# Performance work log

Hardware: AMD Instinct MI355X
Metric: run time of the kernel (lower is better)

## Reference

```python
import jax, jax.numpy as jnp
import numpy as np

H = 32       # num query heads
KVH = 8      # num kv heads
D = 2048     # hidden_dim
B = 2
S = 2048
HD = D // H  # head_dim = 64


def setup_inputs() -> dict:
    key = jax.random.key(0)
    ks = jax.random.split(key, 9)
    s = 1.0 / np.sqrt(D).astype(np.float32)
    kvd = KVH * HD
    x = jax.random.normal(ks[0], (B, S, D), jnp.float32)
    # weights stored as (in, out) so forward is x @ W + b
    Wq = jax.random.normal(ks[1], (D, D), jnp.float32) * s
    bq = jax.random.normal(ks[2], (D,), jnp.float32) * 0.01
    Wk = jax.random.normal(ks[3], (D, kvd), jnp.float32) * s
    bk = jax.random.normal(ks[4], (kvd,), jnp.float32) * 0.01
    Wv = jax.random.normal(ks[5], (D, kvd), jnp.float32) * s
    bv = jax.random.normal(ks[6], (kvd,), jnp.float32) * 0.01
    Wo = jax.random.normal(ks[7], (D, D), jnp.float32) * s
    bo = jax.random.normal(ks[8], (D,), jnp.float32) * 0.01
    return {"x": x, "Wq": Wq, "bq": bq, "Wk": Wk, "bk": bk,
            "Wv": Wv, "bv": bv, "Wo": Wo, "bo": bo}


def reference(x, Wq, bq, Wk, bk, Wv, bv, Wo, bo):
    b, s, d = x.shape
    hd = d // H
    # projections -> (B, heads, S, head_dim)
    Q = (x @ Wq + bq).reshape(b, s, H, hd).transpose(0, 2, 1, 3)
    K = (x @ Wk + bk).reshape(b, s, KVH, hd).transpose(0, 2, 1, 3)
    V = (x @ Wv + bv).reshape(b, s, KVH, hd).transpose(0, 2, 1, 3)
    # GQA: repeat KV heads to match query heads (repeat_interleave on head dim)
    rep = H // KVH
    Kr = jnp.repeat(K, rep, axis=1)
    Vr = jnp.repeat(V, rep, axis=1)
    scale = jnp.asarray(1.0 / np.sqrt(hd), x.dtype)
    scores = jnp.einsum('bhqd,bhkd->bhqk', Q, Kr) * scale
    attn = jax.nn.softmax(scores, axis=-1)
    out = jnp.einsum('bhqk,bhkd->bhqd', attn, Vr)
    out = out.transpose(0, 2, 1, 3).reshape(b, s, d)
    return out @ Wo + bo
```

## Files before the change

### kernel.cpp

```cpp
#include <hip/hip_runtime.h>
#include <hip/hip_bf16.h>
#include <cstdint>

#define NH 32
#define NKVH 8
#define DM 2048
#define NB 2
#define SQ 2048
#define HDIM 64
#define MT (NB*SQ)
#define KVD (NKVH*HDIM)

typedef __attribute__((ext_vector_type(8))) short short8;
typedef __attribute__((ext_vector_type(4))) short short4v;
typedef __attribute__((ext_vector_type(4))) float f32x4;
typedef __attribute__((ext_vector_type(16))) float f32x16;
typedef __attribute__((ext_vector_type(4))) unsigned int uint4v;

static __device__ __forceinline__ short f2b(float f) {
  uint32_t u = __builtin_bit_cast(uint32_t, f);
  u += 0x7FFFu + ((u >> 16) & 1u);
  return (short)(u >> 16);
}

#define GLL16(g, l) __builtin_amdgcn_global_load_lds(                          \
    (__attribute__((address_space(1))) const void*)(g),                        \
    (__attribute__((address_space(3))) void*)(l), 16, 0, 0)

__global__ void cast_x_kernel(const float* __restrict__ x, short* __restrict__ xb, int n4) {
  int i = blockIdx.x * blockDim.x + threadIdx.x;
  const int stride = gridDim.x * blockDim.x;
  for (; i < n4; i += stride) {
    const float4 v = ((const float4*)x)[i];
    short4v o;
    o.x = f2b(v.x); o.y = f2b(v.y); o.z = f2b(v.z); o.w = f2b(v.w);
    ((short4v*)xb)[i] = o;
  }
}

__global__ void transpose_cast_kernel(const float* __restrict__ W, short* __restrict__ Wt,
                                      int Kd, int Nd) {
  __shared__ float tile[32][33];
  const int n0 = blockIdx.x * 32, k0 = blockIdx.y * 32;
  const int tx = threadIdx.x & 31, ty = threadIdx.x >> 5;
#pragma unroll
  for (int i = 0; i < 4; i++)
    tile[ty + i * 8][tx] = W[(size_t)(k0 + ty + i * 8) * Nd + n0 + tx];
  __syncthreads();
#pragma unroll
  for (int i = 0; i < 4; i++)
    Wt[(size_t)(n0 + ty + i * 8) * Kd + k0 + tx] = f2b(tile[tx][ty + i * 8]);
}

template <int EPI>
__global__ __launch_bounds__(256) void gemm_kernel(const short* __restrict__ A,
                                                   const short* __restrict__ Bt,
                                                   const float* __restrict__ bias,
                                                   void* __restrict__ Cout, int N) {
  __shared__ __align__(16) short As[128 * 32];
  __shared__ __align__(16) short Bs[128 * 32];
  const int K = DM;
  const int tid = threadIdx.x;
  const int wave = tid >> 6, lane = tid & 63;
  const int g = lane >> 4, r16 = lane & 15;
  const int m0 = blockIdx.y * 128, n0 = blockIdx.x * 128;
  const int wr = wave >> 1, wc = wave & 1;

  f32x4 acc[4][4];
#pragma unroll
  for (int i = 0; i < 4; i++)
#pragma unroll
    for (int j = 0; j < 4; j++) acc[i][j] = (f32x4){0.f, 0.f, 0.f, 0.f};

  const int srow = lane >> 2, sslot = lane & 3;
  const short* aS0 = A + (size_t)(m0 + (wave * 2 + 0) * 16 + srow) * K + sslot * 8;
  const short* aS1 = A + (size_t)(m0 + (wave * 2 + 1) * 16 + srow) * K + sslot * 8;
  const short* bS0 = Bt + (size_t)(n0 + (wave * 2 + 0) * 16 + srow) * K + sslot * 8;
  const short* bS1 = Bt + (size_t)(n0 + (wave * 2 + 1) * 16 + srow) * K + sslot * 8;
  short* aD0 = As + (wave * 2 + 0) * 512;
  short* aD1 = As + (wave * 2 + 1) * 512;
  short* bD0 = Bs + (wave * 2 + 0) * 512;
  short* bD1 = Bs + (wave * 2 + 1) * 512;

  for (int k0 = 0; k0 < K; k0 += 32) {
    GLL16(aS0 + k0, aD0);
    GLL16(aS1 + k0, aD1);
    GLL16(bS0 + k0, bD0);
    GLL16(bS1 + k0, bD1);
    __syncthreads();
    short8 af[4], bf[4];
#pragma unroll
    for (int mi = 0; mi < 4; mi++)
      af[mi] = *(const short8*)&As[(wr * 64 + mi * 16 + r16) * 32 + g * 8];
#pragma unroll
    for (int ni = 0; ni < 4; ni++)
      bf[ni] = *(const short8*)&Bs[(wc * 64 + ni * 16 + r16) * 32 + g * 8];
#pragma unroll
    for (int mi = 0; mi < 4; mi++)
#pragma unroll
      for (int ni = 0; ni < 4; ni++)
        acc[mi][ni] = __builtin_amdgcn_mfma_f32_16x16x32_bf16(af[mi], bf[ni], acc[mi][ni], 0, 0, 0);
    __syncthreads();
  }

  float bvv[4];
#pragma unroll
  for (int ni = 0; ni < 4; ni++) bvv[ni] = bias[n0 + wc * 64 + ni * 16 + r16];
#pragma unroll
  for (int mi = 0; mi < 4; mi++) {
#pragma unroll
    for (int ni = 0; ni < 4; ni++) {
      const int n = n0 + wc * 64 + ni * 16 + r16;
#pragma unroll
      for (int j = 0; j < 4; j++) {
        const int m = m0 + wr * 64 + mi * 16 + g * 4 + j;
        const float v = acc[mi][ni][j] + bvv[ni];
        if (EPI == 0) {
          ((short*)Cout)[(size_t)m * N + n] = f2b(v);
        } else {
          ((float*)Cout)[(size_t)m * N + n] = v;
        }
      }
    }
  }
}

__global__ __launch_bounds__(256) void gemm_kv_kernel(const short* __restrict__ A,
                                                      const short* __restrict__ Bt,
                                                      const float* __restrict__ bk,
                                                      const float* __restrict__ bv,
                                                      short* __restrict__ Kout,
                                                      short* __restrict__ Vout) {
  __shared__ __align__(16) short As[128 * 32];
  __shared__ __align__(16) short Bs[128 * 32];
  const int K = DM;
  const int tid = threadIdx.x;
  const int wave = tid >> 6, lane = tid & 63;
  const int g = lane >> 4, r16 = lane & 15;
  const int m0 = blockIdx.y * 128, n0 = blockIdx.x * 128;
  const int wr = wave >> 1, wc = wave & 1;

  f32x4 acc[4][4];
#pragma unroll
  for (int i = 0; i < 4; i++)
#pragma unroll
    for (int j = 0; j < 4; j++) acc[i][j] = (f32x4){0.f, 0.f, 0.f, 0.f};

  const int srow = lane >> 2, sslot = lane & 3;
  const short* aS0 = A + (size_t)(m0 + (wave * 2 + 0) * 16 + srow) * K + sslot * 8;
  const short* aS1 = A + (size_t)(m0 + (wave * 2 + 1) * 16 + srow) * K + sslot * 8;
  const short* bS0 = Bt + (size_t)(n0 + (wave * 2 + 0) * 16 + srow) * K + sslot * 8;
  const short* bS1 = Bt + (size_t)(n0 + (wave * 2 + 1) * 16 + srow) * K + sslot * 8;
  short* aD0 = As + (wave * 2 + 0) * 512;
  short* aD1 = As + (wave * 2 + 1) * 512;
  short* bD0 = Bs + (wave * 2 + 0) * 512;
  short* bD1 = Bs + (wave * 2 + 1) * 512;

  for (int k0 = 0; k0 < K; k0 += 32) {
    GLL16(aS0 + k0, aD0);
    GLL16(aS1 + k0, aD1);
    GLL16(bS0 + k0, bD0);
    GLL16(bS1 + k0, bD1);
    __syncthreads();
    short8 af[4], bf[4];
#pragma unroll
    for (int mi = 0; mi < 4; mi++)
      af[mi] = *(const short8*)&As[(wr * 64 + mi * 16 + r16) * 32 + g * 8];
#pragma unroll
    for (int ni = 0; ni < 4; ni++)
      bf[ni] = *(const short8*)&Bs[(wc * 64 + ni * 16 + r16) * 32 + g * 8];
#pragma unroll
    for (int mi = 0; mi < 4; mi++)
#pragma unroll
      for (int ni = 0; ni < 4; ni++)
        acc[mi][ni] = __builtin_amdgcn_mfma_f32_16x16x32_bf16(af[mi], bf[ni], acc[mi][ni], 0, 0, 0);
    __syncthreads();
  }

  const bool isK = (n0 < 512);
  float bvv[4];
#pragma unroll
  for (int ni = 0; ni < 4; ni++) {
    const int n = n0 + wc * 64 + ni * 16 + r16;
    bvv[ni] = isK ? bk[n] : bv[n - 512];
  }
#pragma unroll
  for (int mi = 0; mi < 4; mi++) {
#pragma unroll
    for (int ni = 0; ni < 4; ni++) {
      const int n = n0 + wc * 64 + ni * 16 + r16;
#pragma unroll
      for (int j = 0; j < 4; j++) {
        const int m = m0 + wr * 64 + mi * 16 + g * 4 + j;
        const float v = acc[mi][ni][j] + bvv[ni];
        if (isK) {
          Kout[(size_t)m * KVD + n] = f2b(v);
        } else {
          const int np = n - 512;
          const int bb = m >> 11, s = m & (SQ - 1);
          const int kvh = np >> 6, d = np & 63;
          Vout[((size_t)((bb * NKVH + kvh) * HDIM + d) << 11) + s] = f2b(v);
        }
      }
    }
  }
}

__global__ __launch_bounds__(256, 2) void attn_kernel(const short* __restrict__ Qb,
                                                      const short* __restrict__ Kb,
                                                      const short* __restrict__ Vtb,
                                                      short* __restrict__ Ab) {
  __shared__ __align__(16) short Ks[2][64 * 64];
  __shared__ __align__(16) short Vs[2][64 * 64];
  __shared__ float alds[4][32];

  const int tid = threadIdx.x, wave = tid >> 6, lane = tid & 63;
  const int la31 = lane & 31, hi = lane >> 5;

  const int pb = blockIdx.x;
  const int lb = (pb & 7) * 128 + (pb >> 3);
  const int qb = lb & 15, h = (lb >> 4) & 31, b = lb >> 9;
  const int kvh = h >> 2;

  const float SCL = 0.18033688f;
  const float THR = 44.3614f;

  short8 qf[4];
  {
    const int qrow = b * SQ + qb * 128 + wave * 32 + la31;
    const short* qp = Qb + (size_t)qrow * DM + h * HDIM;
#pragma unroll
    for (int ks = 0; ks < 4; ks++)
      qf[ks] = *(const short8*)(qp + ks * 16 + hi * 8);
  }

  f32x16 o[2];
#pragma unroll
  for (int nt = 0; nt < 2; nt++)
#pragma unroll
    for (int r = 0; r < 16; r++) o[nt][r] = 0.f;
  float m = -1e30f, l = 0.f;

  const int r3 = lane >> 3, sp = lane & 7;
  const int cs = (sp ^ r3) * 8;
  const int krow0 = wave * 16 + r3, krow1 = wave * 16 + 8 + r3;
  const short* kS0 = Kb + (size_t)(b * SQ + krow0) * KVD + kvh * HDIM + cs;
  const short* kS1 = Kb + (size_t)(b * SQ + krow1) * KVD + kvh * HDIM + cs;
  const short* vS0 = Vtb + (size_t)((b * NKVH + kvh) * HDIM + krow0) * SQ + cs;
  const short* vS1 = Vtb + (size_t)((b * NKVH + kvh) * HDIM + krow1) * SQ + cs;
  char* kD0base = (char*)&Ks[0][0] + (wave * 2 + 0) * 1024;
  char* kD1base = (char*)&Ks[0][0] + (wave * 2 + 1) * 1024;
  char* vD0base = (char*)&Vs[0][0] + (wave * 2 + 0) * 1024;
  char* vD1base = (char*)&Vs[0][0] + (wave * 2 + 1) * 1024;

  const int xr = (la31 & 7) << 4;

  GLL16(kS0, kD0base);
  GLL16(kS1, kD1base);
  GLL16(vS0, vD0base);
  GLL16(vS1, vD1base);
  __syncthreads();

  int cur = 0;
  for (int t = 0; t < SQ / 64; t++) {
    if (t + 1 < SQ / 64) {
      const int nxt = cur ^ 1;
      const size_t ko = (size_t)(t + 1) * 64 * KVD;
      const int vo = (t + 1) * 64;
      GLL16(kS0 + ko, kD0base + nxt * 8192);
      GLL16(kS1 + ko, kD1base + nxt * 8192);
      GLL16(vS0 + vo, vD0base + nxt * 8192);
      GLL16(vS1 + vo, vD1base + nxt * 8192);
    }

    f32x16 st[2];
#pragma unroll
    for (int tt = 0; tt < 2; tt++) {
#pragma unroll
      for (int r = 0; r < 16; r++) st[tt][r] = 0.f;
#pragma unroll
      for (int ks = 0; ks < 4; ks++) {
        const short8 kf = *(const short8*)((const char*)&Ks[cur][0] +
            (32 * tt + la31) * 128 + ((32 * ks + 16 * hi) ^ xr));
        st[tt] = __builtin_amdgcn_mfma_f32_32x32x16_bf16(kf, qf[ks], st[tt], 0, 0, 0);
      }
    }

    float t16a[16];
#pragma unroll
    for (int i = 0; i < 16; i++) t16a[i] = fmaxf(st[0][i], st[1][i]);
#pragma unroll
    for (int off = 8; off >= 1; off >>= 1)
#pragma unroll
      for (int i = 0; i < off; i++) t16a[i] = fmaxf(t16a[i], t16a[i + off]);
    float pmax = t16a[0];
    pmax = fmaxf(pmax, __shfl_xor(pmax, 32));

    if (!__all(pmax <= m + THR)) {
      const float mnew = fmaxf(m, pmax);
      const float al = exp2f((m - mnew) * SCL);
      m = mnew;
      l *= al;
      alds[wave][la31] = al;
      asm volatile("s_waitcnt lgkmcnt(0)" ::: "memory");
      f32x4 av[4];
#pragma unroll
      for (int rr = 0; rr < 4; rr++)
        av[rr] = *(const f32x4*)&alds[wave][rr * 8 + hi * 4];
#pragma unroll
      for (int nt = 0; nt < 2; nt++)
#pragma unroll
        for (int r = 0; r < 16; r++) o[nt][r] *= av[r >> 2][r & 3];
    }

    const float nmsc = -m * SCL;
#pragma unroll
    for (int tt = 0; tt < 2; tt++)
#pragma unroll
      for (int r = 0; r < 16; r++)
        st[tt][r] = exp2f(fmaf(st[tt][r], SCL, nmsc));

    {
      float u[16];
#pragma unroll
      for (int i = 0; i < 16; i++) u[i] = st[0][i] + st[1][i];
#pragma unroll
      for (int off = 8; off >= 1; off >>= 1)
#pragma unroll
        for (int i = 0; i < off; i++) u[i] += u[i + off];
      float ps = u[0];
      ps += __shfl_xor(ps, 32);
      l += ps;
    }

    uint32_t pk[16];
#pragma unroll
    for (int tt = 0; tt < 2; tt++)
#pragma unroll
      for (int i = 0; i < 8; i++)
        pk[tt * 8 + i] = ((uint32_t)(uint16_t)f2b(st[tt][2 * i + 1]) << 16) |
                         (uint16_t)f2b(st[tt][2 * i]);

    short8 pa[4];
#pragma unroll
    for (int ks4 = 0; ks4 < 4; ks4++) {
      uint32_t w02[2], w13[2];
#pragma unroll
      for (int pp = 0; pp < 2; pp++) {
        const uint32_t a = pk[ks4 * 4 + pp];
        const uint32_t c = pk[ks4 * 4 + 2 + pp];
        const uint32_t u = hi ? a : c;
        const uint32_t s2 = (uint32_t)__shfl_xor((int)u, 32);
        w02[pp] = hi ? s2 : a;
        w13[pp] = hi ? c : s2;
      }
      uint4v wv;
      wv.x = w02[0]; wv.y = w02[1]; wv.z = w13[0]; wv.w = w13[1];
      pa[ks4] = __builtin_bit_cast(short8, wv);
    }

#pragma unroll
    for (int nt = 0; nt < 2; nt++)
#pragma unroll
      for (int ks = 0; ks < 4; ks++) {
        const short8 vf = *(const short8*)((const char*)&Vs[cur][0] +
            (32 * nt + la31) * 128 + ((32 * ks + 16 * hi) ^ xr));
        o[nt] = __builtin_amdgcn_mfma_f32_32x32x16_bf16(pa[ks], vf, o[nt], 0, 0, 0);
      }

    __syncthreads();
    cur ^= 1;
  }

  alds[wave][la31] = l;
  asm volatile("s_waitcnt lgkmcnt(0)" ::: "memory");
  float inv[16];
#pragma unroll
  for (int rr = 0; rr < 4; rr++) {
    const f32x4 lv = *(const f32x4*)&alds[wave][rr * 8 + hi * 4];
#pragma unroll
    for (int j = 0; j < 4; j++) inv[rr * 4 + j] = 1.0f / lv[j];
  }
  const int orow = b * SQ + qb * 128 + wave * 32;
#pragma unroll
  for (int nt = 0; nt < 2; nt++)
#pragma unroll
    for (int r = 0; r < 16; r++) {
      const int q = (r & 3) + 8 * (r >> 2) + 4 * hi;
      Ab[(size_t)(orow + q) * DM + h * HDIM + nt * 32 + la31] =
          f2b(o[nt][r] * inv[(r >> 2) * 4 + (r & 3)]);
    }
}

extern "C" void kernel_launch(void* const* d_in, const int* in_sizes, int n_in,
                              void* d_out, int out_size, void* d_ws, size_t ws_size,
                              hipStream_t stream) {
  const float* x  = (const float*)d_in[0];
  const float* Wq = (const float*)d_in[1];
  const float* bq = (const float*)d_in[2];
  const float* Wk = (const float*)d_in[3];
  const float* bk = (const float*)d_in[4];
  const float* Wv = (const float*)d_in[5];
  const float* bv = (const float*)d_in[6];
  const float* Wo = (const float*)d_in[7];
  const float* bo = (const float*)d_in[8];

  short* ws = (short*)d_ws;
  size_t off = 0;
  short* xb  = ws + off; off += (size_t)MT * DM;
  short* Wqt = ws + off; off += (size_t)DM * DM;
  short* Wkt = ws + off; off += (size_t)KVD * DM;
  short* Wvt = ws + off; off += (size_t)KVD * DM;
  short* Wot = ws + off; off += (size_t)DM * DM;
  short* Qb  = ws + off; off += (size_t)MT * DM;
  short* Kb  = ws + off; off += (size_t)MT * KVD;
  short* Vtb = ws + off; off += (size_t)MT * KVD;
  short* Ab  = ws + off;

  cast_x_kernel<<<2048, 256, 0, stream>>>(x, xb, MT * DM / 4);
  transpose_cast_kernel<<<dim3(DM / 32, DM / 32), 256, 0, stream>>>(Wq, Wqt, DM, DM);
  transpose_cast_kernel<<<dim3(KVD / 32, DM / 32), 256, 0, stream>>>(Wk, Wkt, DM, KVD);
  transpose_cast_kernel<<<dim3(KVD / 32, DM / 32), 256, 0, stream>>>(Wv, Wvt, DM, KVD);
  transpose_cast_kernel<<<dim3(DM / 32, DM / 32), 256, 0, stream>>>(Wo, Wot, DM, DM);

  gemm_kernel<0><<<dim3(DM / 128, MT / 128), 256, 0, stream>>>(xb, Wqt, bq, Qb, DM);
  gemm_kv_kernel<<<dim3(1024 / 128, MT / 128), 256, 0, stream>>>(xb, Wkt, bk, bv, Kb, Vtb);

  attn_kernel<<<NB * NH * (SQ / 128), 256, 0, stream>>>(Qb, Kb, Vtb, Ab);

  gemm_kernel<2><<<dim3(DM / 128, MT / 128), 256, 0, stream>>>(Ab, Wot, bo, d_out, DM);
}
```

Before: 419.3 us.

## Double-buffer GEMM LDS tiles, add setprio around MFMA, use packed bf16 convert

The projection GEMMs now double-buffer their LDS tiles, prefetching the next K-slice with global_load_lds while computing the current one. This removes one barrier per iteration and overlaps load latency with MFMA work. s_setprio raises wave priority around MFMA blocks in both the GEMM and attention kernels. In attention, the row-max reduction is rewritten as a flatter tree, and P is packed with the hardware v_cvt_pk_bf16_f32 instruction instead of software rounding. Double buffering doubles LDS use per block, which may lower occupancy, and the hardware convert's rounding may differ slightly from the manual f2b.

Result: faster. 395.5 us (-5.7%).

```diff
diff --git a/kernel.cpp b/kernel.cpp
--- a/kernel.cpp
+++ b/kernel.cpp
@@ -23,6 +23,12 @@
   return (short)(u >> 16);
 }
 
+static __device__ __forceinline__ uint32_t cvt_pk_bf16(float lo, float hi) {
+  uint32_t r;
+  asm("v_cvt_pk_bf16_f32 %0, %1, %2" : "=v"(r) : "v"(lo), "v"(hi));
+  return r;
+}
+
 #define GLL16(g, l) __builtin_amdgcn_global_load_lds(                          \
     (__attribute__((address_space(1))) const void*)(g),                        \
     (__attribute__((address_space(3))) void*)(l), 16, 0, 0)
@@ -57,8 +63,8 @@
                                                    const short* __restrict__ Bt,
                                                    const float* __restrict__ bias,
                                                    void* __restrict__ Cout, int N) {
-  __shared__ __align__(16) short As[128 * 32];
-  __shared__ __align__(16) short Bs[128 * 32];
+  __shared__ __align__(16) short As[2 * 128 * 32];
+  __shared__ __align__(16) short Bs[2 * 128 * 32];
   const int K = DM;
   const int tid = threadIdx.x;
   const int wave = tid >> 6, lane = tid & 63;
@@ -82,25 +88,39 @@
   short* bD0 = Bs + (wave * 2 + 0) * 512;
   short* bD1 = Bs + (wave * 2 + 1) * 512;
 
+  GLL16(aS0, aD0);
+  GLL16(aS1, aD1);
+  GLL16(bS0, bD0);
+  GLL16(bS1, bD1);
+  __syncthreads();
+
+  int buf = 0;
   for (int k0 = 0; k0 < K; k0 += 32) {
-    GLL16(aS0 + k0, aD0);
-    GLL16(aS1 + k0, aD1);
-    GLL16(bS0 + k0, bD0);
-    GLL16(bS1 + k0, bD1);
-    __syncthreads();
+    if (k0 + 32 < K) {
+      const int nb2 = (buf ^ 1) * 4096;
+      GLL16(aS0 + k0 + 32, aD0 + nb2);
+      GLL16(aS1 + k0 + 32, aD1 + nb2);
+      GLL16(bS0 + k0 + 32, bD0 + nb2);
+      GLL16(bS1 + k0 + 32, bD1 + nb2);
+    }
+    const short* Ac = As + buf * 4096;
+    const short* Bc = Bs + buf * 4096;
     short8 af[4], bf[4];
 #pragma unroll
     for (int mi = 0; mi < 4; mi++)
-      af[mi] = *(const short8*)&As[(wr * 64 + mi * 16 + r16) * 32 + g * 8];
+      af[mi] = *(const short8*)&Ac[(wr * 64 + mi * 16 + r16) * 32 + g * 8];
 #pragma unroll
     for (int ni = 0; ni < 4; ni++)
-      bf[ni] = *(const short8*)&Bs[(wc * 64 + ni * 16 + r16) * 32 + g * 8];
+      bf[ni] = *(const short8*)&Bc[(wc * 64 + ni * 16 + r16) * 32 + g * 8];
+    __builtin_amdgcn_s_setprio(1);
 #pragma unroll
     for (int mi = 0; mi < 4; mi++)
 #pragma unroll
       for (int ni = 0; ni < 4; ni++)
         acc[mi][ni] = __builtin_amdgcn_mfma_f32_16x16x32_bf16(af[mi], bf[ni], acc[mi][ni], 0, 0, 0);
+    __builtin_amdgcn_s_setprio(0);
     __syncthreads();
+    buf ^= 1;
   }
 
   float bvv[4];
@@ -131,8 +151,8 @@
                                                       const float* __restrict__ bv,
                                                       short* __restrict__ Kout,
                                                       short* __restrict__ Vout) {
-  __shared__ __align__(16) short As[128 * 32];
-  __shared__ __align__(16) short Bs[128 * 32];
+  __shared__ __align__(16) short As[2 * 128 * 32];
+  __shared__ __align__(16) short Bs[2 * 128 * 32];
   const int K = DM;
   const int tid = threadIdx.x;
   const int wave = tid >> 6, lane = tid & 63;
@@ -156,25 +176,39 @@
   short* bD0 = Bs + (wave * 2 + 0) * 512;
   short* bD1 = Bs + (wave * 2 + 1) * 512;
 
+  GLL16(aS0, aD0);
+  GLL16(aS1, aD1);
+  GLL16(bS0, bD0);
+  GLL16(bS1, bD1);
+  __syncthreads();
+
+  int buf = 0;
   for (int k0 = 0; k0 < K; k0 += 32) {
-    GLL16(aS0 + k0, aD0);
-    GLL16(aS1 + k0, aD1);
-    GLL16(bS0 + k0, bD0);
-    GLL16(bS1 + k0, bD1);
-    __syncthreads();
+    if (k0 + 32 < K) {
+      const int nb2 = (buf ^ 1) * 4096;
+      GLL16(aS0 + k0 + 32, aD0 + nb2);
+      GLL16(aS1 + k0 + 32, aD1 + nb2);
+      GLL16(bS0 + k0 + 32, bD0 + nb2);
+      GLL16(bS1 + k0 + 32, bD1 + nb2);
+    }
+    const short* Ac = As + buf * 4096;
+    const short* Bc = Bs + buf * 4096;
     short8 af[4], bf[4];
 #pragma unroll
     for (int mi = 0; mi < 4; mi++)
-      af[mi] = *(const short8*)&As[(wr * 64 + mi * 16 + r16) * 32 + g * 8];
+      af[mi] = *(const short8*)&Ac[(wr * 64 + mi * 16 + r16) * 32 + g * 8];
 #pragma unroll
     for (int ni = 0; ni < 4; ni++)
-      bf[ni] = *(const short8*)&Bs[(wc * 64 + ni * 16 + r16) * 32 + g * 8];
+      bf[ni] = *(const short8*)&Bc[(wc * 64 + ni * 16 + r16) * 32 + g * 8];
+    __builtin_amdgcn_s_setprio(1);
 #pragma unroll
     for (int mi = 0; mi < 4; mi++)
 #pragma unroll
       for (int ni = 0; ni < 4; ni++)
         acc[mi][ni] = __builtin_amdgcn_mfma_f32_16x16x32_bf16(af[mi], bf[ni], acc[mi][ni], 0, 0, 0);
+    __builtin_amdgcn_s_setprio(0);
     __syncthreads();
+    buf ^= 1;
   }
 
   const bool isK = (n0 < 512);
@@ -278,22 +312,27 @@
     for (int tt = 0; tt < 2; tt++) {
 #pragma unroll
       for (int r = 0; r < 16; r++) st[tt][r] = 0.f;
+      __builtin_amdgcn_s_setprio(1);
 #pragma unroll
       for (int ks = 0; ks < 4; ks++) {
         const short8 kf = *(const short8*)((const char*)&Ks[cur][0] +
             (32 * tt + la31) * 128 + ((32 * ks + 16 * hi) ^ xr));
         st[tt] = __builtin_amdgcn_mfma_f32_32x32x16_bf16(kf, qf[ks], st[tt], 0, 0, 0);
       }
-    }
-
-    float t16a[16];
-#pragma unroll
-    for (int i = 0; i < 16; i++) t16a[i] = fmaxf(st[0][i], st[1][i]);
-#pragma unroll
-    for (int off = 8; off >= 1; off >>= 1)
-#pragma unroll
-      for (int i = 0; i < off; i++) t16a[i] = fmaxf(t16a[i], t16a[i + off]);
-    float pmax = t16a[0];
+      __builtin_amdgcn_s_setprio(0);
+    }
+
+    float c16[16];
+#pragma unroll
+    for (int i = 0; i < 16; i++) c16[i] = fmaxf(st[0][i], st[1][i]);
+    const float t0 = fmaxf(fmaxf(c16[0], c16[1]), c16[2]);
+    const float t1 = fmaxf(fmaxf(c16[3], c16[4]), c16[5]);
+    const float t2 = fmaxf(fmaxf(c16[6], c16[7]), c16[8]);
+    const float t3 = fmaxf(fmaxf(c16[9], c16[10]), c16[11]);
+    const float t4 = fmaxf(fmaxf(c16[12], c16[13]), c16[14]);
+    const float u0 = fmaxf(fmaxf(t0, t1), c16[15]);
+    const float u1 = fmaxf(fmaxf(t2, t3), t4);
+    float pmax = fmaxf(u0, u1);
     pmax = fmaxf(pmax, __shfl_xor(pmax, 32));
 
     if (!__all(pmax <= m + THR)) {
@@ -338,8 +377,7 @@
     for (int tt = 0; tt < 2; tt++)
 #pragma unroll
       for (int i = 0; i < 8; i++)
-        pk[tt * 8 + i] = ((uint32_t)(uint16_t)f2b(st[tt][2 * i + 1]) << 16) |
-                         (uint16_t)f2b(st[tt][2 * i]);
+        pk[tt * 8 + i] = cvt_pk_bf16(st[tt][2 * i], st[tt][2 * i + 1]);
 
     short8 pa[4];
 #pragma unroll
@@ -359,6 +397,7 @@
       pa[ks4] = __builtin_bit_cast(short8, wv);
     }
 
+    __builtin_amdgcn_s_setprio(1);
 #pragma unroll
     for (int nt = 0; nt < 2; nt++)
 #pragma unroll
@@ -367,6 +406,7 @@
             (32 * nt + la31) * 128 + ((32 * ks + 16 * hi) ^ xr));
         o[nt] = __builtin_amdgcn_mfma_f32_32x32x16_bf16(pa[ks], vf, o[nt], 0, 0, 0);
       }
+    __builtin_amdgcn_s_setprio(0);
 
     __syncthreads();
     cur ^= 1;
```
